# Performance work log

Hardware: AMD Instinct MI355X
Metric: run time of the kernel (lower is better)

The kernel has to match this reference:

```python
import jax, jax.numpy as jnp
import numpy as np
import math

B, N, DIM, NH, K, PD = 2, 2048, 512, 8, 32, 16
HD = DIM // NH
LN_EPS = 1e-6  # flax LayerNorm default


def _poincare_dist(x, y, c):
    # x, y broadcast to [B, N, N, PD]; returns [B, N, N]
    diff_norm_sq = jnp.sum((x - y) ** 2, axis=-1)
    x_norm_sq = jnp.sum(x ** 2, axis=-1)
    y_norm_sq = jnp.sum(y ** 2, axis=-1)
    den = (1.0 - c * x_norm_sq) * (1.0 - c * y_norm_sq)
    arg = 1.0 + 2.0 * c * diff_norm_sq / jnp.clip(den, 1e-8)
    safe_arg = jnp.maximum(arg, 1.0 + 1e-7)
    return jnp.arccosh(safe_arg) / jnp.sqrt(c)


def _layernorm(x, scale, bias):
    m = jnp.mean(x, axis=-1, keepdims=True)
    v = jnp.var(x, axis=-1, keepdims=True)
    return (x - m) / jnp.sqrt(v + LN_EPS) * scale + bias


def setup_inputs() -> dict:
    key = jax.random.key(0)
    ks = jax.random.split(key, 12)

    def dense(k, din, dout):
        W = jax.random.normal(k, (din, dout), jnp.float32) / np.sqrt(din).astype(np.float32)
        b = jnp.zeros((dout,), jnp.float32)
        return W, b

    inp = {}
    inp["x"] = jax.random.normal(ks[0], (B, N, DIM), jnp.float32)
    # points inside the unit Poincare ball (c=1)
    inp["positions"] = (jax.random.uniform(ks[1], (B, N, PD), jnp.float32) - 0.5) * 0.2
    inp["c"] = jnp.float32(1.0)
    inp["Wq"], inp["bq"] = dense(ks[2], DIM, DIM)
    inp["Wk"], inp["bk"] = dense(ks[3], DIM, DIM)
    inp["Wv"], inp["bv"] = dense(ks[4], DIM, DIM)
    inp["Wo"], inp["bo"] = dense(ks[5], DIM, DIM)
    inp["W1"], inp["b1"] = dense(ks[6], DIM, 4 * DIM)
    inp["W2"], inp["b2"] = dense(ks[7], 4 * DIM, DIM)
    inp["ln1_scale"] = jnp.ones((DIM,), jnp.float32)
    inp["ln1_bias"] = jnp.zeros((DIM,), jnp.float32)
    inp["ln2_scale"] = jnp.ones((DIM,), jnp.float32)
    inp["ln2_bias"] = jnp.zeros((DIM,), jnp.float32)
    inp["log_tau"] = jnp.zeros((1,), jnp.float32)
    inp["attn_scale"] = jnp.ones((1,), jnp.float32)
    return inp


def reference(x, positions, c, Wq, bq, Wk, bk, Wv, bv, Wo, bo,
              W1, b1, W2, b2, ln1_scale, ln1_bias, ln2_scale, ln2_bias,
              log_tau, attn_scale):
    x_res = x
    x_norm = _layernorm(x, ln1_scale, ln1_bias)

    def heads(W, b):
        return (x_norm @ W + b).reshape(B, N, NH, HD).transpose(0, 2, 1, 3)  # [B,H,N,HD]

    q = heads(Wq, bq)
    k = heads(Wk, bk)
    v = heads(Wv, bv)

    # pairwise hyperbolic distances [B,N,N]
    dist_matrix = _poincare_dist(positions[:, None, :, :], positions[:, :, None, :], c)
    _, top_k_indices = jax.lax.top_k(-dist_matrix, K)  # [B,N,K]

    # gather neighbor K/V: out[b,h,i,j,d] = kv[b,h, idx[b,i,j], d]
    gather = jax.vmap(lambda kv_b, idx_b: kv_b[:, idx_b, :])
    k_gathered = gather(k, top_k_indices)  # [B,H,N,K,HD]
    v_gathered = gather(v, top_k_indices)  # [B,H,N,K,HD]

    feature_scores = jnp.einsum('bhid,bhikd->bhik', q, k_gathered) / math.sqrt(HD)
    gathered_dists = jnp.take_along_axis(dist_matrix, top_k_indices, axis=-1)  # [B,N,K]
    geometric_scores = -gathered_dists[:, None, :, :] / jnp.clip(jnp.exp(log_tau), 1e-8)
    attn_scores = attn_scale * jnp.tanh(feature_scores + geometric_scores)
    attn_weights = jax.nn.softmax(attn_scores, axis=-1)

    attn_output = jnp.einsum('bhik,bhikd->bhid', attn_weights, v_gathered)
    attn_output = attn_output.transpose(0, 2, 1, 3).reshape(B, N, DIM)

    x1 = x_res + attn_output @ Wo + bo
    x2_norm = _layernorm(x1, ln2_scale, ln2_bias)
    ffn = jax.nn.gelu(x2_norm @ W1 + b1) @ W2 + b2  # gelu approximate=True (flax default)
    return x1 + ffn
```

## Files before the change

kernel.cpp:

```cpp
#include <hip/hip_runtime.h>
#include <math.h>

#define B_   2
#define N_   2048
#define DIM_ 512
#define NH_  8
#define HD_  64
#define K_   32
#define PD_  16
#define TOK_ (B_*N_)
#define FFN_ 2048
#define QKV_ (3*DIM_)
#define KV_  1024

typedef __bf16 bf16x8 __attribute__((ext_vector_type(8)));
typedef float  f32x4  __attribute__((ext_vector_type(4)));

__device__ __forceinline__ unsigned short f2bf(float f) {
    unsigned int u = __float_as_uint(f);
    u = (u + 0x7fffu + ((u >> 16) & 1u)) >> 16;
    return (unsigned short)u;
}

__device__ __forceinline__ float bflo(unsigned u) { return __uint_as_float(u << 16); }
__device__ __forceinline__ float bfhi(unsigned u) { return __uint_as_float(u & 0xffff0000u); }

__device__ __forceinline__ float gelu_tanh(float x) {
    float x3 = x * x * x;
    return 0.5f * x * (1.f + tanhf(0.7978845608028654f * (x + 0.044715f * x3)));
}

__device__ __forceinline__ float tanh_fast(float x) {
    float e = __expf(2.f * x);
    return 1.f - 2.f / (e + 1.f);
}

__device__ __forceinline__ int lane_mbcnt(unsigned long long m) {
    return __builtin_amdgcn_mbcnt_hi((unsigned)(m >> 32),
           __builtin_amdgcn_mbcnt_lo((unsigned)m, 0));
}

#define GLOAD_LDS16(g, l) __builtin_amdgcn_global_load_lds(                        \
    (const __attribute__((address_space(1))) unsigned int*)(const void*)(g),       \
    (__attribute__((address_space(3))) unsigned int*)(void*)(l), 16, 0, 0)

template<int EPI, int BM, int BN>
__global__ __launch_bounds__(256)
void gemm_bf16_kernel(const unsigned short* __restrict__ A,
                      const unsigned short* __restrict__ Bt,
                      const float* __restrict__ bias,
                      const float* __restrict__ res,
                      float* __restrict__ Cf,
                      unsigned short* __restrict__ Cb,
                      int N, int Kd)
{
    constexpr int WM = BM / 2;
    constexpr int WN = BN / 2;
    constexpr int FM = WM / 16;
    constexpr int FN = WN / 16;
    constexpr int BUFSZ = (BM + BN) * 64;

    __shared__ __align__(16) unsigned short smem[2 * BUFSZ];

    int t    = threadIdx.x;
    int lane = t & 63;
    int wid  = t >> 6;
    int wm   = wid >> 1, wn = wid & 1;
    int bm0  = blockIdx.y * BM;
    int bn0  = blockIdx.x * BN;
    int quad = lane >> 4;
    int rlo  = lane & 15;

    f32x4 acc[FM][FN] = {};

    auto stage = [&](int buf, int k0) {
        unsigned short* As_ = smem + buf * BUFSZ;
        unsigned short* Bs_ = As_ + BM * 64;
#pragma unroll
        for (int l = 0; l < BM/32; l++) {
            int idx = l*256 + t;
            int r   = idx >> 3;
            int g   = (idx & 7) ^ (r & 7);
            GLOAD_LDS16(A + (size_t)(bm0 + r) * Kd + k0 + g*8, As_ + idx*8);
        }
#pragma unroll
        for (int l = 0; l < BN/32; l++) {
            int idx = l*256 + t;
            int r   = idx >> 3;
            int g   = (idx & 7) ^ (r & 7);
            GLOAD_LDS16(Bt + (size_t)(bn0 + r) * Kd + k0 + g*8, Bs_ + idx*8);
        }
    };

    auto compute = [&](int buf) {
        unsigned short* As_ = smem + buf * BUFSZ;
        unsigned short* Bs_ = As_ + BM * 64;
        bf16x8 af[FM][2], bfr[FN][2];
#pragma unroll
        for (int mi = 0; mi < FM; mi++) {
            int r = wm*WM + mi*16 + rlo;
#pragma unroll
            for (int s = 0; s < 2; s++)
                af[mi][s] = *(const bf16x8*)(As_ + r*64 + ((s*4 + quad) ^ (r & 7))*8);
        }
#pragma unroll
        for (int ni = 0; ni < FN; ni++) {
            int r = wn*WN + ni*16 + rlo;
#pragma unroll
            for (int s = 0; s < 2; s++)
                bfr[ni][s] = *(const bf16x8*)(Bs_ + r*64 + ((s*4 + quad) ^ (r & 7))*8);
        }
#pragma unroll
        for (int s = 0; s < 2; s++)
#pragma unroll
            for (int mi = 0; mi < FM; mi++)
#pragma unroll
                for (int ni = 0; ni < FN; ni++)
                    acc[mi][ni] = __builtin_amdgcn_mfma_f32_16x16x32_bf16(
                        af[mi][s], bfr[ni][s], acc[mi][ni], 0, 0, 0);
    };

    stage(0, 0);
    int buf = 0;
    for (int k0 = 0; k0 < Kd; k0 += 64) {
        __syncthreads();
        if (k0 + 64 < Kd) stage(buf ^ 1, k0 + 64);
        compute(buf);
        buf ^= 1;
    }

#pragma unroll
    for (int mi = 0; mi < FM; mi++) {
#pragma unroll
        for (int ni = 0; ni < FN; ni++) {
            int col = bn0 + wn*WN + ni*16 + rlo;
            float bv = bias[col];
#pragma unroll
            for (int r = 0; r < 4; r++) {
                int row = bm0 + wm*WM + mi*16 + quad*4 + r;
                float val = acc[mi][ni][r] + bv;
                if (EPI == 1) val += res[(size_t)row * N + col];
                if (EPI == 2) {
                    val = gelu_tanh(val);
                    Cb[(size_t)row * N + col] = f2bf(val);
                } else if (EPI == 3) {
                    if (col < DIM_) Cf[(size_t)row * DIM_ + col] = val;
                    else            Cb[(size_t)row * KV_ + (col - DIM_)] = f2bf(val);
                } else {
                    Cf[(size_t)row * N + col] = val;
                }
            }
        }
    }
}

__device__ __forceinline__ void extract_row(const unsigned* rb, unsigned T,
                                            int cnt_lt, int m,
                                            unsigned long long* crow,
                                            int hw, int jbase, int lane)
{
    int ltpos = 0;
#pragma unroll
    for (int tt = 0; tt < 16; tt++) {
        bool is_lt = rb[tt] < T;
        unsigned long long mlt = __ballot(is_lt);
        int p = ltpos + lane_mbcnt(mlt);
        if (is_lt) {
            int j = jbase + (tt >> 2)*256 + lane*4 + (tt & 3);
            crow[hw*K_ + p] = ((unsigned long long)rb[tt] << 32) | (unsigned)j;
        }
        ltpos += __popcll(mlt);
    }
    int eqpos = 0;
#pragma unroll
    for (int jg = 0; jg < 4; jg++) {
        bool iseq[4]; unsigned long long meq[4]; int bel[4];
#pragma unroll
        for (int jj = 0; jj < 4; jj++) {
            iseq[jj] = (rb[jg*4+jj] == T);
            meq[jj]  = __ballot(iseq[jj]);
            bel[jj]  = lane_mbcnt(meq[jj]);
        }
        int lane_prefix = bel[0] + bel[1] + bel[2] + bel[3];
        int within = 0;
#pragma unroll
        for (int jj = 0; jj < 4; jj++) {
            int p = eqpos + lane_prefix + within;
            if (iseq[jj] && p < m) {
                int j = jbase + jg*256 + lane*4 + jj;
                crow[hw*K_ + cnt_lt + p] =
                    ((unsigned long long)rb[jg*4+jj] << 32) | (unsigned)j;
            }
            within += iseq[jj] ? 1 : 0;
        }
        eqpos += __popcll(meq[0]) + __popcll(meq[1]) + __popcll(meq[2]) + __popcll(meq[3]);
    }
}

__global__ __launch_bounds__(256)
void dist_topk_kernel(const float* __restrict__ pos,
                      const float* __restrict__ posT,
                      const float* __restrict__ pos_sq,
                      const float* __restrict__ c_ptr,
                      int* __restrict__ topk_idx, float* __restrict__ topk_dist)
{
    __shared__ unsigned long long cand[4][64];

    int wid  = threadIdx.x >> 6;
    int lane = threadIdx.x & 63;
    int rg   = wid >> 1;
    int hw   = wid & 1;
    int bi0  = blockIdx.x * 4 + rg * 2;
    int b    = bi0 >> 11;
    float c  = *c_ptr;
    float inv_sqrt_c = rsqrtf(c);

    float pi0[16], pi1[16];
    {
        const float4* q0 = (const float4*)(pos + (size_t)bi0 * PD_);
        const float4* q1 = (const float4*)(pos + (size_t)(bi0+1) * PD_);
#pragma unroll
        for (int u = 0; u < 4; u++) {
            float4 a = q0[u];
            pi0[4*u]=a.x; pi0[4*u+1]=a.y; pi0[4*u+2]=a.z; pi0[4*u+3]=a.w;
            float4 e = q1[u];
            pi1[4*u]=e.x; pi1[4*u+1]=e.y; pi1[4*u+2]=e.z; pi1[4*u+3]=e.w;
        }
    }
    float om0 = 1.f - c * pos_sq[bi0];
    float om1 = 1.f - c * pos_sq[bi0+1];

    const float* pT  = posT + (size_t)b * 16 * N_;
    const float* sqb = pos_sq + b * N_;
    int jbase = hw * 1024;
    int j0l   = jbase + lane * 4;

    unsigned rb0[16], rb1[16];
#pragma unroll
    for (int jg = 0; jg < 4; jg++) {
        int j0 = j0l + jg * 256;
        float ax=0,ay=0,az=0,aw=0, bx=0,by=0,bz=0,bw=0;
#pragma unroll
        for (int d = 0; d < 16; d++) {
            float4 v = *(const float4*)(pT + d * N_ + j0);
            float d0x = pi0[d]-v.x, d0y = pi0[d]-v.y, d0z = pi0[d]-v.z, d0w = pi0[d]-v.w;
            ax += d0x*d0x; ay += d0y*d0y; az += d0z*d0z; aw += d0w*d0w;
            float d1x = pi1[d]-v.x, d1y = pi1[d]-v.y, d1z = pi1[d]-v.z, d1w = pi1[d]-v.w;
            bx += d1x*d1x; by += d1y*d1y; bz += d1z*d1z; bw += d1w*d1w;
        }
        float4 sq = *(const float4*)(sqb + j0);
        float da[4]={ax,ay,az,aw}, db[4]={bx,by,bz,bw}, sqa[4]={sq.x,sq.y,sq.z,sq.w};
#pragma unroll
        for (int jj = 0; jj < 4; jj++) {
            float omj  = 1.f - c * sqa[jj];
            float den0 = fmaxf(om0 * omj, 1e-8f);
            float den1 = fmaxf(om1 * omj, 1e-8f);
            rb0[jg*4+jj] = __float_as_uint(fmaxf(1.f + 2.f*c*da[jj]/den0, 1.f+1e-7f));
            rb1[jg*4+jj] = __float_as_uint(fmaxf(1.f + 2.f*c*db[jj]/den1, 1.f+1e-7f));
        }
    }

    unsigned T0, T1;
    {
        unsigned band0 = rb0[0], bor0 = rb0[0], band1 = rb1[0], bor1 = rb1[0];
#pragma unroll
        for (int tt = 1; tt < 16; tt++) {
            band0 &= rb0[tt]; bor0 |= rb0[tt];
            band1 &= rb1[tt]; bor1 |= rb1[tt];
        }
#pragma unroll
        for (int off = 32; off; off >>= 1) {
            band0 &= __shfl_xor(band0, off); bor0 |= __shfl_xor(bor0, off);
            band1 &= __shfl_xor(band1, off); bor1 |= __shfl_xor(bor1, off);
        }
        unsigned df0 = band0 ^ bor0, df1 = band1 ^ bor1;
        int hib0 = df0 ? (31 - __clz(df0)) : -1;
        int hib1 = df1 ? (31 - __clz(df1)) : -1;
        int hib  = hib0 > hib1 ? hib0 : hib1;
        T0 = (hib >= 0) ? (band0 & ~((1u << (hib+1)) - 1u)) : band0;
        T1 = (hib >= 0) ? (band1 & ~((1u << (hib+1)) - 1u)) : band1;
        for (int bit = hib; bit >= 0; --bit) {
            unsigned p0 = T0 | (1u << bit), p1 = T1 | (1u << bit);
            int c0 = 0, c1 = 0;
#pragma unroll
            for (int tt = 0; tt < 16; tt++) {
                c0 += __popcll(__ballot(rb0[tt] < p0));
                c1 += __popcll(__ballot(rb1[tt] < p1));
            }
            if (c0 < K_) T0 = p0;
            if (c1 < K_) T1 = p1;
        }
    }
    int cl0 = 0, cl1 = 0;
#pragma unroll
    for (int tt = 0; tt < 16; tt++) {
        cl0 += __popcll(__ballot(rb0[tt] < T0));
        cl1 += __popcll(__ballot(rb1[tt] < T1));
    }

    extract_row(rb0, T0, cl0, K_ - cl0, cand[rg*2+0], hw, jbase, lane);
    extract_row(rb1, T1, cl1, K_ - cl1, cand[rg*2+1], hw, jbase, lane);
    __syncthreads();

    {
        unsigned long long mykey = cand[wid][lane];
        int rank = 0;
#pragma unroll 8
        for (int M = 0; M < 64; M++)
            rank += (cand[wid][M] < mykey) ? 1 : 0;
        if (rank < K_) {
            int bi = blockIdx.x * 4 + wid;
            topk_idx [(size_t)bi * K_ + rank] = (int)(mykey & 0xffffffffu);
            topk_dist[(size_t)bi * K_ + rank] =
                acoshf(__uint_as_float((unsigned)(mykey >> 32))) * inv_sqrt_c;
        }
    }
}

__global__ void fused_prep_kernel(const float* __restrict__ Wq, const float* __restrict__ Wk,
                            const float* __restrict__ Wv, const float* __restrict__ Wo,
                            const float* __restrict__ W1, const float* __restrict__ W2,
                            const float* __restrict__ bq, const float* __restrict__ bk,
                            const float* __restrict__ bv,
                            unsigned short* __restrict__ qkvWt,
                            unsigned short* __restrict__ WoT,
                            unsigned short* __restrict__ W1T,
                            unsigned short* __restrict__ W2T,
                            float* __restrict__ qkv_b,
                            const float* __restrict__ pos,
                            float* __restrict__ pos_sq,
                            float* __restrict__ posT,
                            const float* __restrict__ x,
                            const float* __restrict__ ln1_scale,
                            const float* __restrict__ ln1_bias,
                            unsigned short* __restrict__ xn)
{
    int id = blockIdx.x;
    int t  = threadIdx.x;

    if (id >= 3094) {
        int wave = (id - 3094) * 4 + (t >> 6);
        int lane = t & 63;
        const float* xr = x + (size_t)wave * DIM_;
        float v[8];
        float s = 0.f;
#pragma unroll
        for (int i = 0; i < 8; i++) { v[i] = xr[lane + i*64]; s += v[i]; }
#pragma unroll
        for (int off = 32; off; off >>= 1) s += __shfl_xor(s, off);
        float mean = s * (1.f / DIM_);
        float vs = 0.f;
#pragma unroll
        for (int i = 0; i < 8; i++) { float d = v[i] - mean; vs += d*d; }
#pragma unroll
        for (int off = 32; off; off >>= 1) vs += __shfl_xor(vs, off);
        float inv = rsqrtf(vs * (1.f / DIM_) + 1e-6f);
        unsigned short* yr = xn + (size_t)wave * DIM_;
#pragma unroll
        for (int i = 0; i < 8; i++) {
            int cc = lane + i*64;
            yr[cc] = f2bf((v[i] - mean) * inv * ln1_scale[cc] + ln1_bias[cc]);
        }
        return;
    }
    if (id >= 3078) {
        int i = (id - 3078) * 256 + t;
        int b = i >> 11, j = i & (N_ - 1);
        const float4* p = (const float4*)(pos + (size_t)i * PD_);
        float4 a0 = p[0], a1 = p[1], a2 = p[2], a3 = p[3];
        float pv[16] = {a0.x,a0.y,a0.z,a0.w, a1.x,a1.y,a1.z,a1.w,
                        a2.x,a2.y,a2.z,a2.w, a3.x,a3.y,a3.z,a3.w};
        float s = 0.f;
#pragma unroll
        for (int d = 0; d < 16; d++) s += pv[d]*pv[d];
        pos_sq[i] = s;
        float* pT = posT + (size_t)b * 16 * N_;
#pragma unroll
        for (int d = 0; d < 16; d++) pT[d * N_ + j] = pv[d];
        return;
    }
    if (id >= 3072) {
        int i = (id - 3072) * 256 + t;
        if (i < DIM_)            qkv_b[i] = bq[i];
        else if (i < 2*DIM_)     qkv_b[i] = bk[i - DIM_];
        else                     qkv_b[i] = bv[i - 2*DIM_];
        return;
    }

    const float* W; unsigned short* Wt; int Kd, Nw, nx, ti;
    if      (id < 256)  { W = Wq; Wt = qkvWt;               Kd = 512;  Nw = 512;  nx = 16; ti = id; }
    else if (id < 512)  { W = Wk; Wt = qkvWt + 512*512;     Kd = 512;  Nw = 512;  nx = 16; ti = id - 256; }
    else if (id < 768)  { W = Wv; Wt = qkvWt + 2*512*512;   Kd = 512;  Nw = 512;  nx = 16; ti = id - 512; }
    else if (id < 1024) { W = Wo; Wt = WoT;                 Kd = 512;  Nw = 512;  nx = 16; ti = id - 768; }
    else if (id < 2048) { W = W1; Wt = W1T;                 Kd = 512;  Nw = 2048; nx = 64; ti = id - 1024; }
    else                { W = W2; Wt = W2T;                 Kd = 2048; Nw = 512;  nx = 16; ti = id - 2048; }

    __shared__ float tile[32][33];
    int n0 = (ti % nx) * 32, k0 = (ti / nx) * 32;
    int tx = t & 31, ty = t >> 5;
#pragma unroll
    for (int i = 0; i < 32; i += 8)
        tile[ty + i][tx] = W[(size_t)(k0 + ty + i) * Nw + n0 + tx];
    __syncthreads();
#pragma unroll
    for (int i = 0; i < 32; i += 8)
        Wt[(size_t)(n0 + ty + i) * Kd + k0 + tx] = f2bf(tile[tx][ty + i]);
}

__global__ void layernorm_kernel(const float* __restrict__ x,
                                 const float* __restrict__ scale,
                                 const float* __restrict__ bias,
                                 unsigned short* __restrict__ y)
{
    int wave = (blockIdx.x * blockDim.x + threadIdx.x) >> 6;
    int lane = threadIdx.x & 63;
    if (wave >= TOK_) return;
    const float* xr = x + (size_t)wave * DIM_;
    float v[8];
    float s = 0.f;
#pragma unroll
    for (int i = 0; i < 8; i++) { v[i] = xr[lane + i*64]; s += v[i]; }
#pragma unroll
    for (int off = 32; off; off >>= 1) s += __shfl_xor(s, off);
    float mean = s * (1.f / DIM_);
    float vs = 0.f;
#pragma unroll
    for (int i = 0; i < 8; i++) { float d = v[i] - mean; vs += d*d; }
#pragma unroll
    for (int off = 32; off; off >>= 1) vs += __shfl_xor(vs, off);
    float inv = rsqrtf(vs * (1.f / DIM_) + 1e-6f);
    unsigned short* yr = y + (size_t)wave * DIM_;
#pragma unroll
    for (int i = 0; i < 8; i++) {
        int c = lane + i*64;
        yr[c] = f2bf((v[i] - mean) * inv * scale[c] + bias[c]);
    }
}

__global__ __launch_bounds__(256)
void attn_kernel(const float* __restrict__ q,
                 const unsigned short* __restrict__ kv,
                 const int* __restrict__ topk_idx, const float* __restrict__ topk_dist,
                 const float* __restrict__ log_tau_p, const float* __restrict__ attn_scale_p,
                 unsigned int* __restrict__ out)
{
    int gw   = (blockIdx.x * blockDim.x + threadIdx.x) >> 6;
    int lane = threadIdx.x & 63;
    if (gw >= B_ * NH_ * N_) return;
    int b = gw / (NH_ * N_);
    int r = gw % (NH_ * N_);
    int h = r / N_;
    int i = r % N_;
    int tok = b * N_ + i;

    float tau    = fmaxf(__expf(*log_tau_p), 1e-8f);
    float ascale = *attn_scale_p;

    const int*   idxp = topk_idx  + (size_t)tok * K_;
    const float* dstp = topk_dist + (size_t)tok * K_;
    int   my_idx  = idxp[lane & 31];
    float my_dist = dstp[lane & 31];

    int jj   = lane >> 1;
    int half = lane & 1;

    const float4* qp = (const float4*)(q + (size_t)tok * DIM_ + h * HD_ + half * 32);
    float4 qv[8];
#pragma unroll
    for (int u = 0; u < 8; u++) qv[u] = qp[u];

    int nb = __shfl(my_idx, jj);
    const uint4* kp = (const uint4*)(kv + (size_t)(b * N_ + nb) * KV_ + h * HD_ + half * 32);
    float dot = 0.f;
#pragma unroll
    for (int u = 0; u < 4; u++) {
        uint4 kw = kp[u];
        dot += qv[2*u].x   * bflo(kw.x) + qv[2*u].y   * bfhi(kw.x)
             + qv[2*u].z   * bflo(kw.y) + qv[2*u].w   * bfhi(kw.y)
             + qv[2*u+1].x * bflo(kw.z) + qv[2*u+1].y * bfhi(kw.z)
             + qv[2*u+1].z * bflo(kw.w) + qv[2*u+1].w * bfhi(kw.w);
    }
    dot += __shfl_xor(dot, 1);

    float fs = dot * 0.125f;
    float gs = -__shfl(my_dist, jj) / tau;
    float s  = ascale * tanh_fast(fs + gs);

    float mx = s;
#pragma unroll
    for (int off = 32; off; off >>= 1) mx = fmaxf(mx, __shfl_xor(mx, off));
    float e  = __expf(s - mx);
    float ec = half ? 0.f : e;
#pragma unroll
    for (int off = 32; off; off >>= 1) ec += __shfl_xor(ec, off);
    float inv = 1.f / ec;

    int dp    = lane & 31;
    int half2 = lane >> 5;
    const unsigned int* vb = (const unsigned int*)(kv + DIM_ + h * HD_) + dp;
    float ax = 0.f, ay = 0.f;
#pragma unroll
    for (int it = 0; it < 16; it++) {
        int t2 = half2 + 2*it;
        float w  = __shfl(e, t2 * 2) * inv;
        int   nj = __shfl(my_idx, t2);
        unsigned vv = vb[(size_t)(b * N_ + nj) * (KV_/2)];
        ax += w * bflo(vv);
        ay += w * bfhi(vv);
    }
    ax += __shfl_xor(ax, 32);
    ay += __shfl_xor(ay, 32);
    if (lane < 32) {
        unsigned pck = ((unsigned)f2bf(ay) << 16) | (unsigned)f2bf(ax);
        out[(size_t)tok * (DIM_/2) + h * (HD_/2) + dp] = pck;
    }
}

extern "C" void kernel_launch(void* const* d_in, const int* in_sizes, int n_in,
                              void* d_out, int out_size, void* d_ws, size_t ws_size,
                              hipStream_t stream)
{
    const float* x          = (const float*)d_in[0];
    const float* positions  = (const float*)d_in[1];
    const float* c_p        = (const float*)d_in[2];
    const float* Wq         = (const float*)d_in[3];
    const float* bq         = (const float*)d_in[4];
    const float* Wk         = (const float*)d_in[5];
    const float* bk         = (const float*)d_in[6];
    const float* Wv         = (const float*)d_in[7];
    const float* bv         = (const float*)d_in[8];
    const float* Wo         = (const float*)d_in[9];
    const float* bo         = (const float*)d_in[10];
    const float* W1         = (const float*)d_in[11];
    const float* b1         = (const float*)d_in[12];
    const float* W2         = (const float*)d_in[13];
    const float* b2         = (const float*)d_in[14];
    const float* ln1_scale  = (const float*)d_in[15];
    const float* ln1_bias   = (const float*)d_in[16];
    const float* ln2_scale  = (const float*)d_in[17];
    const float* ln2_bias   = (const float*)d_in[18];
    const float* log_tau    = (const float*)d_in[19];
    const float* attn_scale = (const float*)d_in[20];

    char* p = (char*)d_ws;
    unsigned short* qkvWt  = (unsigned short*)p; p += (size_t)QKV_ * DIM_ * 2;
    unsigned short* WoT    = (unsigned short*)p; p += (size_t)DIM_ * DIM_ * 2;
    unsigned short* W1T    = (unsigned short*)p; p += (size_t)FFN_ * DIM_ * 2;
    unsigned short* W2T    = (unsigned short*)p; p += (size_t)DIM_ * FFN_ * 2;
    float*          qkv_b  = (float*)p;          p += (size_t)QKV_ * 4;
    unsigned short* xn     = (unsigned short*)p; p += (size_t)TOK_ * DIM_ * 2;
    float*          qf     = (float*)p;          p += (size_t)TOK_ * DIM_ * 4;
    unsigned short* kvb    = (unsigned short*)p; p += (size_t)TOK_ * KV_ * 2;
    unsigned short* attn_o = (unsigned short*)p; p += (size_t)TOK_ * DIM_ * 2;
    float*          x1     = (float*)p;          p += (size_t)TOK_ * DIM_ * 4;
    unsigned short* x2n    = (unsigned short*)p; p += (size_t)TOK_ * DIM_ * 2;
    unsigned short* hbuf   = (unsigned short*)p; p += (size_t)TOK_ * FFN_ * 2;
    float*          pos_sq = (float*)p;          p += (size_t)TOK_ * 4;
    float*          posT   = (float*)p;          p += (size_t)B_ * 16 * N_ * 4;
    float*          tk_d   = (float*)p;          p += (size_t)TOK_ * K_ * 4;
    int*            tk_i   = (int*)p;            p += (size_t)TOK_ * K_ * 4;

    fused_prep_kernel<<<4118, 256, 0, stream>>>(Wq, Wk, Wv, Wo, W1, W2, bq, bk, bv,
                                                qkvWt, WoT, W1T, W2T, qkv_b,
                                                positions, pos_sq, posT,
                                                x, ln1_scale, ln1_bias, xn);

    gemm_bf16_kernel<3,64,128><<<dim3(QKV_/128, TOK_/64), 256, 0, stream>>>(
        xn, qkvWt, qkv_b, nullptr, qf, kvb, QKV_, DIM_);

    dist_topk_kernel<<<TOK_/4, 256, 0, stream>>>(positions, posT, pos_sq,
                                                 c_p, tk_i, tk_d);

    attn_kernel<<<(B_*NH_*N_)/4, 256, 0, stream>>>(qf, kvb, tk_i, tk_d,
                                                   log_tau, attn_scale,
                                                   (unsigned int*)attn_o);

    gemm_bf16_kernel<1,64,64><<<dim3(DIM_/64, TOK_/64), 256, 0, stream>>>(
        attn_o, WoT, bo, x, x1, nullptr, DIM_, DIM_);

    layernorm_kernel<<<TOK_/4, 256, 0, stream>>>(x1, ln2_scale, ln2_bias, x2n);

    gemm_bf16_kernel<2,64,128><<<dim3(FFN_/128, TOK_/64), 256, 0, stream>>>(
        x2n, W1T, b1, nullptr, nullptr, hbuf, FFN_, DIM_);

    gemm_bf16_kernel<1,64,64><<<dim3(DIM_/64, TOK_/64), 256, 0, stream>>>(
        hbuf, W2T, b2, x1, (float*)d_out, nullptr, DIM_, FFN_);
}
```

Before: 254.0 us.

## Split top-k rows across four waves and resolve two threshold bits per step

Each block now handles two query rows, with all four waves splitting the 2048 candidates into 512-wide slices, instead of two row pairs each split across two waves. This halves per-thread register arrays and the per-pass ballot work, and doubles the grid. The radix threshold search now tests three candidate thresholds per iteration to resolve two bits at once, halving the serial loop depth at the cost of more ballots per step. The final merge ranks 128 candidates per row instead of 64.

Result: faster. 243.9 us (-4.0%).

```diff
diff --git a/kernel.cpp b/kernel.cpp
--- a/kernel.cpp
+++ b/kernel.cpp
@@ -154,26 +154,27 @@
     }
 }
 
+template<int NR>
 __device__ __forceinline__ void extract_row(const unsigned* rb, unsigned T,
                                             int cnt_lt, int m,
                                             unsigned long long* crow,
-                                            int hw, int jbase, int lane)
+                                            int part, int jbase, int lane)
 {
     int ltpos = 0;
 #pragma unroll
-    for (int tt = 0; tt < 16; tt++) {
+    for (int tt = 0; tt < NR; tt++) {
         bool is_lt = rb[tt] < T;
         unsigned long long mlt = __ballot(is_lt);
         int p = ltpos + lane_mbcnt(mlt);
         if (is_lt) {
             int j = jbase + (tt >> 2)*256 + lane*4 + (tt & 3);
-            crow[hw*K_ + p] = ((unsigned long long)rb[tt] << 32) | (unsigned)j;
+            crow[part*K_ + p] = ((unsigned long long)rb[tt] << 32) | (unsigned)j;
         }
         ltpos += __popcll(mlt);
     }
     int eqpos = 0;
 #pragma unroll
-    for (int jg = 0; jg < 4; jg++) {
+    for (int jg = 0; jg < NR/4; jg++) {
         bool iseq[4]; unsigned long long meq[4]; int bel[4];
 #pragma unroll
         for (int jj = 0; jj < 4; jj++) {
@@ -188,7 +189,7 @@
             int p = eqpos + lane_prefix + within;
             if (iseq[jj] && p < m) {
                 int j = jbase + jg*256 + lane*4 + jj;
-                crow[hw*K_ + cnt_lt + p] =
+                crow[part*K_ + cnt_lt + p] =
                     ((unsigned long long)rb[jg*4+jj] << 32) | (unsigned)j;
             }
             within += iseq[jj] ? 1 : 0;
@@ -204,13 +205,11 @@
                       const float* __restrict__ c_ptr,
                       int* __restrict__ topk_idx, float* __restrict__ topk_dist)
 {
-    __shared__ unsigned long long cand[4][64];
+    __shared__ unsigned long long cand[2][128];
 
     int wid  = threadIdx.x >> 6;
     int lane = threadIdx.x & 63;
-    int rg   = wid >> 1;
-    int hw   = wid & 1;
-    int bi0  = blockIdx.x * 4 + rg * 2;
+    int bi0  = blockIdx.x * 2;
     int b    = bi0 >> 11;
     float c  = *c_ptr;
     float inv_sqrt_c = rsqrtf(c);
@@ -232,12 +231,12 @@
 
     const float* pT  = posT + (size_t)b * 16 * N_;
     const float* sqb = pos_sq + b * N_;
-    int jbase = hw * 1024;
+    int jbase = wid * 512;
     int j0l   = jbase + lane * 4;
 
-    unsigned rb0[16], rb1[16];
-#pragma unroll
-    for (int jg = 0; jg < 4; jg++) {
+    unsigned rb0[8], rb1[8];
+#pragma unroll
+    for (int jg = 0; jg < 2; jg++) {
         int j0 = j0l + jg * 256;
         float ax=0,ay=0,az=0,aw=0, bx=0,by=0,bz=0,bw=0;
 #pragma unroll
@@ -264,7 +263,7 @@
     {
         unsigned band0 = rb0[0], bor0 = rb0[0], band1 = rb1[0], bor1 = rb1[0];
 #pragma unroll
-        for (int tt = 1; tt < 16; tt++) {
+        for (int tt = 1; tt < 8; tt++) {
             band0 &= rb0[tt]; bor0 |= rb0[tt];
             band1 &= rb1[tt]; bor1 |= rb1[tt];
         }
@@ -279,11 +278,30 @@
         int hib  = hib0 > hib1 ? hib0 : hib1;
         T0 = (hib >= 0) ? (band0 & ~((1u << (hib+1)) - 1u)) : band0;
         T1 = (hib >= 0) ? (band1 & ~((1u << (hib+1)) - 1u)) : band1;
-        for (int bit = hib; bit >= 0; --bit) {
-            unsigned p0 = T0 | (1u << bit), p1 = T1 | (1u << bit);
+        int bit = hib;
+        while (bit >= 1) {
+            unsigned lo = 1u << (bit - 1);
+            unsigned p01 = T0 | lo, p02 = T0 | (lo << 1), p03 = T0 | (lo*3u);
+            unsigned p11 = T1 | lo, p12 = T1 | (lo << 1), p13 = T1 | (lo*3u);
+            int c01=0,c02=0,c03=0,c11=0,c12=0,c13=0;
+#pragma unroll
+            for (int tt = 0; tt < 8; tt++) {
+                c01 += __popcll(__ballot(rb0[tt] < p01));
+                c02 += __popcll(__ballot(rb0[tt] < p02));
+                c03 += __popcll(__ballot(rb0[tt] < p03));
+                c11 += __popcll(__ballot(rb1[tt] < p11));
+                c12 += __popcll(__ballot(rb1[tt] < p12));
+                c13 += __popcll(__ballot(rb1[tt] < p13));
+            }
+            T0 = (c03 < K_) ? p03 : (c02 < K_) ? p02 : (c01 < K_) ? p01 : T0;
+            T1 = (c13 < K_) ? p13 : (c12 < K_) ? p12 : (c11 < K_) ? p11 : T1;
+            bit -= 2;
+        }
+        if (bit == 0) {
+            unsigned p0 = T0 | 1u, p1 = T1 | 1u;
             int c0 = 0, c1 = 0;
 #pragma unroll
-            for (int tt = 0; tt < 16; tt++) {
+            for (int tt = 0; tt < 8; tt++) {
                 c0 += __popcll(__ballot(rb0[tt] < p0));
                 c1 += __popcll(__ballot(rb1[tt] < p1));
             }
@@ -293,23 +311,24 @@
     }
     int cl0 = 0, cl1 = 0;
 #pragma unroll
-    for (int tt = 0; tt < 16; tt++) {
+    for (int tt = 0; tt < 8; tt++) {
         cl0 += __popcll(__ballot(rb0[tt] < T0));
         cl1 += __popcll(__ballot(rb1[tt] < T1));
     }
 
-    extract_row(rb0, T0, cl0, K_ - cl0, cand[rg*2+0], hw, jbase, lane);
-    extract_row(rb1, T1, cl1, K_ - cl1, cand[rg*2+1], hw, jbase, lane);
+    extract_row<8>(rb0, T0, cl0, K_ - cl0, cand[0], wid, jbase, lane);
+    extract_row<8>(rb1, T1, cl1, K_ - cl1, cand[1], wid, jbase, lane);
     __syncthreads();
 
     {
-        unsigned long long mykey = cand[wid][lane];
+        int row  = wid >> 1, half = wid & 1;
+        unsigned long long mykey = cand[row][half*64 + lane];
         int rank = 0;
 #pragma unroll 8
-        for (int M = 0; M < 64; M++)
-            rank += (cand[wid][M] < mykey) ? 1 : 0;
+        for (int M = 0; M < 128; M++)
+            rank += (cand[row][M] < mykey) ? 1 : 0;
         if (rank < K_) {
-            int bi = blockIdx.x * 4 + wid;
+            int bi = bi0 + row;
             topk_idx [(size_t)bi * K_ + rank] = (int)(mykey & 0xffffffffu);
             topk_dist[(size_t)bi * K_ + rank] =
                 acoshf(__uint_as_float((unsigned)(mykey >> 32))) * inv_sqrt_c;
@@ -568,7 +587,7 @@
     gemm_bf16_kernel<3,64,128><<<dim3(QKV_/128, TOK_/64), 256, 0, stream>>>(
         xn, qkvWt, qkv_b, nullptr, qf, kvb, QKV_, DIM_);
 
-    dist_topk_kernel<<<TOK_/4, 256, 0, stream>>>(positions, posT, pos_sq,
+    dist_topk_kernel<<<TOK_/2, 256, 0, stream>>>(positions, posT, pos_sq,
                                                  c_p, tk_i, tk_d);
 
     attn_kernel<<<(B_*NH_*N_)/4, 256, 0, stream>>>(qf, kvb, tk_i, tk_d,
```
